# Performance work log

Hardware: AMD Instinct MI355X
Metric: run time of the kernel (lower is better)

## Reference

```python
import jax, jax.numpy as jnp
import numpy as np

B, H, N, D = 4, 16, 2048, 64


def setup_inputs() -> dict:
    key = jax.random.key(0)
    kq, kk, kv, km, kb = jax.random.split(key, 5)
    q = jax.random.normal(kq, (B, H, N, D), dtype=jnp.float32)
    k = jax.random.normal(kk, (B, H, N, D), dtype=jnp.float32)
    v = jax.random.normal(kv, (B, H, N, D), dtype=jnp.float32)
    # mostly-True mask so no row is fully masked
    mask = jax.random.uniform(km, (B, 1, N, N)) > 0.1
    attn_bias = jax.random.normal(kb, (1, H, N, N), dtype=jnp.float32)
    return {"q": q, "k": k, "v": v, "mask": mask, "attn_bias": attn_bias}


def reference(q, k, v, mask, attn_bias):
    scale = q.shape[-1] ** -0.5
    # sim: [B,H,N,N]
    sim = jnp.einsum('bhid,bhjd->bhij', q, k) * scale
    sim = sim + attn_bias
    neg = -jnp.finfo(sim.dtype).max
    sim = jnp.where(mask, sim, neg)
    attn = jax.nn.softmax(sim, axis=-1)
    out = jnp.einsum('bhij,bhjd->bhid', attn, v)
    return out
```

## Files before the change

### kernel.cpp

```cpp
#include <hip/hip_runtime.h>
#include <hip/hip_bf16.h>

typedef __bf16 bf16_t;
typedef bf16_t bf16x8 __attribute__((ext_vector_type(8)));
typedef float  floatx4 __attribute__((ext_vector_type(4)));

constexpr int Bb = 4, Hh = 16, Nn = 2048, Dd = 64;
constexpr int BM = 128;
constexpr int BN = 64;
constexpr int WM = 16;
constexpr float SCALE = 0.125f;
constexpr float NEG   = -3.4028234663852886e38f;

__global__ __launch_bounds__(512, 4)
void attn_fwd(const float* __restrict__ qg,
              const float* __restrict__ kg,
              const float* __restrict__ vg,
              const void*  __restrict__ maskg,
              const float* __restrict__ biasg,
              float* __restrict__ outg)
{
    __shared__ bf16x8 k_lds[512];
    __shared__ bf16x8 v_lds[512];
    __shared__ bf16x8 p_lds[8][128];

    const int tid  = threadIdx.x;
    const int wave = tid >> 6;
    const int lane = tid & 63;
    const int ln   = lane & 15;
    const int lq   = lane >> 4;

    const int id = blockIdx.x;
    const int b  = id & 3;
    const int h  = (id >> 2) & 15;
    const int mt = id >> 6;

    const int probe = ((const int*)maskg)[lane];
    const bool mask_i32 = __all(probe == 0 || probe == 1);
    const int*           mi = (const int*)maskg;
    const unsigned char* mb = (const unsigned char*)maskg;

    const size_t head  = (size_t)(b*Hh + h) * Nn * Dd;
    const int    qbase = mt*BM + wave*WM;

    bf16x8 qa[2];
    {
        const float* qp = qg + head + (size_t)(qbase + ln)*Dd + lq*8;
        #pragma unroll
        for (int kk = 0; kk < 2; ++kk) {
            float4 f0 = *(const float4*)(qp + kk*32);
            float4 f1 = *(const float4*)(qp + kk*32 + 4);
            bf16x8 a;
            a[0]=(bf16_t)f0.x; a[1]=(bf16_t)f0.y; a[2]=(bf16_t)f0.z; a[3]=(bf16_t)f0.w;
            a[4]=(bf16_t)f1.x; a[5]=(bf16_t)f1.y; a[6]=(bf16_t)f1.z; a[7]=(bf16_t)f1.w;
            qa[kk] = a;
        }
    }

    floatx4 o_acc[4];
    #pragma unroll
    for (int i = 0; i < 4; ++i) o_acc[i] = (floatx4){0.f,0.f,0.f,0.f};
    float mx[4], lsum[4];
    #pragma unroll
    for (int r = 0; r < 4; ++r) { mx[r] = -__builtin_inff(); lsum[r] = 0.f; }

    const int skey = tid >> 3;
    const int sd0  = (tid & 7) * 8;
    const int sblk = skey >> 4, sn = skey & 15;
    const int kkg  = sd0 >> 5,  qg2 = (sd0 >> 3) & 3;
    const int vkk  = skey >> 5, vq = (skey >> 3) & 3, vj = skey & 7;
    const int vnb  = sd0 >> 4;
    bf16_t* vl = (bf16_t*)v_lds;
    bf16_t* pl = (bf16_t*)p_lds[wave];

    for (int kt = 0; kt < Nn/BN; ++kt) {
        __syncthreads();
        {
            const float* kp = kg + head + (size_t)(kt*BN + skey)*Dd + sd0;
            const float* vp = vg + head + (size_t)(kt*BN + skey)*Dd + sd0;
            float4 k0 = *(const float4*)(kp);
            float4 k1 = *(const float4*)(kp + 4);
            float4 v0 = *(const float4*)(vp);
            float4 v1 = *(const float4*)(vp + 4);
            bf16x8 c;
            c[0]=(bf16_t)k0.x; c[1]=(bf16_t)k0.y; c[2]=(bf16_t)k0.z; c[3]=(bf16_t)k0.w;
            c[4]=(bf16_t)k1.x; c[5]=(bf16_t)k1.y; c[6]=(bf16_t)k1.z; c[7]=(bf16_t)k1.w;
            k_lds[(sblk*2 + kkg)*64 + qg2*16 + sn] = c;
            float vvv[8];
            *(float4*)(vvv)   = v0;
            *(float4*)(vvv+4) = v1;
            #pragma unroll
            for (int t = 0; t < 8; ++t) {
                const int nn2 = (sd0 & 8) + t;
                vl[(((vkk*4 + vnb)*64 + vq*16 + nn2) << 3) | vj] = (bf16_t)vvv[t];
            }
        }
        __syncthreads();

        floatx4 s_acc[4];
        #pragma unroll
        for (int i = 0; i < 4; ++i) s_acc[i] = (floatx4){0.f,0.f,0.f,0.f};
        #pragma unroll
        for (int blk = 0; blk < 4; ++blk)
            #pragma unroll
            for (int kk = 0; kk < 2; ++kk)
                s_acc[blk] = __builtin_amdgcn_mfma_f32_16x16x32_bf16(
                    qa[kk], k_lds[(blk*2+kk)*64 + lane], s_acc[blk], 0, 0, 0);

        float sv[4][4], rmax[4];
        const size_t col0 = (size_t)kt*BN + ln;
        #pragma unroll
        for (int r = 0; r < 4; ++r) {
            const int m = qbase + lq*4 + r;
            const size_t brow = ((size_t)h*Nn + m)*Nn + col0;
            const size_t mrow = ((size_t)b*Nn + m)*Nn + col0;
            rmax[r] = NEG;
            #pragma unroll
            for (int blk = 0; blk < 4; ++blk) {
                float val = s_acc[blk][r]*SCALE + biasg[brow + blk*16];
                const bool ok = mask_i32 ? (mi[mrow + blk*16] != 0)
                                         : (mb[mrow + blk*16] != 0);
                val = ok ? val : NEG;
                sv[r][blk] = val;
                rmax[r] = fmaxf(rmax[r], val);
            }
        }
        #pragma unroll
        for (int off = 1; off < 16; off <<= 1)
            #pragma unroll
            for (int r = 0; r < 4; ++r)
                rmax[r] = fmaxf(rmax[r], __shfl_xor(rmax[r], off, 64));

        float alph[4], rsum[4];
        bf16_t pb[4][4];
        #pragma unroll
        for (int r = 0; r < 4; ++r) {
            const float mnew = fmaxf(mx[r], rmax[r]);
            alph[r] = __expf(mx[r] - mnew);
            mx[r] = mnew;
            float s = 0.f;
            #pragma unroll
            for (int blk = 0; blk < 4; ++blk) {
                const bf16_t p = (bf16_t)__expf(sv[r][blk] - mnew);
                pb[r][blk] = p;
                s += (float)p;
            }
            rsum[r] = s;
        }
        #pragma unroll
        for (int off = 1; off < 16; off <<= 1)
            #pragma unroll
            for (int r = 0; r < 4; ++r)
                rsum[r] += __shfl_xor(rsum[r], off, 64);
        #pragma unroll
        for (int r = 0; r < 4; ++r) {
            lsum[r] = lsum[r]*alph[r] + rsum[r];
            #pragma unroll
            for (int nb = 0; nb < 4; ++nb)
                o_acc[nb][r] *= alph[r];
        }

        #pragma unroll
        for (int r = 0; r < 4; ++r) {
            const int m = lq*4 + r;
            #pragma unroll
            for (int blk = 0; blk < 4; ++blk) {
                const int key = blk*16 + ln;
                const int kk2 = key >> 5, q2 = (key >> 3) & 3, j2 = key & 7;
                pl[((kk2*64 + q2*16 + m) << 3) | j2] = pb[r][blk];
            }
        }

        #pragma unroll
        for (int kk = 0; kk < 2; ++kk) {
            const bf16x8 pa = p_lds[wave][kk*64 + lane];
            #pragma unroll
            for (int nb = 0; nb < 4; ++nb)
                o_acc[nb] = __builtin_amdgcn_mfma_f32_16x16x32_bf16(
                    pa, v_lds[(kk*4+nb)*64 + lane], o_acc[nb], 0, 0, 0);
        }
    }

    #pragma unroll
    for (int r = 0; r < 4; ++r) {
        const int m = qbase + lq*4 + r;
        const float inv = 1.f / lsum[r];
        float* op = outg + head + (size_t)m*Dd + ln;
        #pragma unroll
        for (int nb = 0; nb < 4; ++nb)
            op[nb*16] = o_acc[nb][r] * inv;
    }
}

extern "C" void kernel_launch(void* const* d_in, const int* in_sizes, int n_in,
                              void* d_out, int out_size, void* d_ws, size_t ws_size,
                              hipStream_t stream) {
    const float* q    = (const float*)d_in[0];
    const float* k    = (const float*)d_in[1];
    const float* v    = (const float*)d_in[2];
    const void*  mask = d_in[3];
    const float* bias = (const float*)d_in[4];
    float* out = (float*)d_out;
    (void)in_sizes; (void)n_in; (void)out_size; (void)d_ws; (void)ws_size;

    const int grid = Bb * Hh * (Nn / BM);
    attn_fwd<<<grid, 512, 0, stream>>>(q, k, v, mask, bias, out);
}
```

Baseline: 1.015 ms.

## Double-buffer K/V in LDS and prefetch next tile's bias and mask into registers

K/V tiles now live in two LDS buffers. The next tile's K/V values are loaded into registers right after the barrier, so the per-iteration leading __syncthreads goes away. The bias and mask values for the next key tile are also loaded and combined one iteration ahead, so their global-memory latency overlaps the softmax and PV MFMA work. The probabilities are written to LDS inside the exp loop, which removes the separate pb array. The cost is more live registers per thread at 512 threads per block, which may affect occupancy or cause spills.

Measured after the change: 1.074 ms. 5.8% more time.

```diff
diff --git a/kernel.cpp b/kernel.cpp
--- a/kernel.cpp
+++ b/kernel.cpp
@@ -9,6 +9,7 @@
 constexpr int BM = 128;
 constexpr int BN = 64;
 constexpr int WM = 16;
+constexpr int NT = Nn / BN;
 constexpr float SCALE = 0.125f;
 constexpr float NEG   = -3.4028234663852886e38f;
 
@@ -20,8 +21,8 @@
               const float* __restrict__ biasg,
               float* __restrict__ outg)
 {
-    __shared__ bf16x8 k_lds[512];
-    __shared__ bf16x8 v_lds[512];
+    __shared__ bf16x8 k_lds[2][512];
+    __shared__ bf16x8 v_lds[2][512];
     __shared__ bf16x8 p_lds[8][128];
 
     const int tid  = threadIdx.x;
@@ -70,25 +71,45 @@
     const int kkg  = sd0 >> 5,  qg2 = (sd0 >> 3) & 3;
     const int vkk  = skey >> 5, vq = (skey >> 3) & 3, vj = skey & 7;
     const int vnb  = sd0 >> 4;
-    bf16_t* vl = (bf16_t*)v_lds;
     bf16_t* pl = (bf16_t*)p_lds[wave];
 
-    for (int kt = 0; kt < Nn/BN; ++kt) {
-        __syncthreads();
+    const float* kbase = kg + head + (size_t)skey*Dd + sd0;
+    const float* vbase = vg + head + (size_t)skey*Dd + sd0;
+
+    float4 kr0 = *(const float4*)(kbase);
+    float4 kr1 = *(const float4*)(kbase + 4);
+    float4 vr0 = *(const float4*)(vbase);
+    float4 vr1 = *(const float4*)(vbase + 4);
+
+    float bias_pf[4][4];
+    {
+        const size_t col0 = (size_t)ln;
+        #pragma unroll
+        for (int r = 0; r < 4; ++r) {
+            const int m = qbase + lq*4 + r;
+            const size_t brow = ((size_t)h*Nn + m)*Nn + col0;
+            const size_t mrow = ((size_t)b*Nn + m)*Nn + col0;
+            #pragma unroll
+            for (int blk = 0; blk < 4; ++blk) {
+                const bool ok = mask_i32 ? (mi[mrow + blk*16] != 0)
+                                         : (mb[mrow + blk*16] != 0);
+                bias_pf[r][blk] = ok ? biasg[brow + blk*16] : NEG;
+            }
+        }
+    }
+
+    for (int kt = 0; kt < NT; ++kt) {
+        const int cur = kt & 1;
+
         {
-            const float* kp = kg + head + (size_t)(kt*BN + skey)*Dd + sd0;
-            const float* vp = vg + head + (size_t)(kt*BN + skey)*Dd + sd0;
-            float4 k0 = *(const float4*)(kp);
-            float4 k1 = *(const float4*)(kp + 4);
-            float4 v0 = *(const float4*)(vp);
-            float4 v1 = *(const float4*)(vp + 4);
             bf16x8 c;
-            c[0]=(bf16_t)k0.x; c[1]=(bf16_t)k0.y; c[2]=(bf16_t)k0.z; c[3]=(bf16_t)k0.w;
-            c[4]=(bf16_t)k1.x; c[5]=(bf16_t)k1.y; c[6]=(bf16_t)k1.z; c[7]=(bf16_t)k1.w;
-            k_lds[(sblk*2 + kkg)*64 + qg2*16 + sn] = c;
+            c[0]=(bf16_t)kr0.x; c[1]=(bf16_t)kr0.y; c[2]=(bf16_t)kr0.z; c[3]=(bf16_t)kr0.w;
+            c[4]=(bf16_t)kr1.x; c[5]=(bf16_t)kr1.y; c[6]=(bf16_t)kr1.z; c[7]=(bf16_t)kr1.w;
+            k_lds[cur][(sblk*2 + kkg)*64 + qg2*16 + sn] = c;
             float vvv[8];
-            *(float4*)(vvv)   = v0;
-            *(float4*)(vvv+4) = v1;
+            *(float4*)(vvv)   = vr0;
+            *(float4*)(vvv+4) = vr1;
+            bf16_t* vl = (bf16_t*)v_lds[cur];
             #pragma unroll
             for (int t = 0; t < 8; ++t) {
                 const int nn2 = (sd0 & 8) + t;
@@ -97,6 +118,15 @@
         }
         __syncthreads();
 
+        if (kt + 1 < NT) {
+            const float* kp = kbase + (size_t)(kt+1)*BN*Dd;
+            const float* vp = vbase + (size_t)(kt+1)*BN*Dd;
+            kr0 = *(const float4*)(kp);
+            kr1 = *(const float4*)(kp + 4);
+            vr0 = *(const float4*)(vp);
+            vr1 = *(const float4*)(vp + 4);
+        }
+
         floatx4 s_acc[4];
         #pragma unroll
         for (int i = 0; i < 4; ++i) s_acc[i] = (floatx4){0.f,0.f,0.f,0.f};
@@ -105,23 +135,16 @@
             #pragma unroll
             for (int kk = 0; kk < 2; ++kk)
                 s_acc[blk] = __builtin_amdgcn_mfma_f32_16x16x32_bf16(
-                    qa[kk], k_lds[(blk*2+kk)*64 + lane], s_acc[blk], 0, 0, 0);
-
-        float sv[4][4], rmax[4];
-        const size_t col0 = (size_t)kt*BN + ln;
-        #pragma unroll
-        for (int r = 0; r < 4; ++r) {
-            const int m = qbase + lq*4 + r;
-            const size_t brow = ((size_t)h*Nn + m)*Nn + col0;
-            const size_t mrow = ((size_t)b*Nn + m)*Nn + col0;
+                    qa[kk], k_lds[cur][(blk*2+kk)*64 + lane], s_acc[blk], 0, 0, 0);
+
+        float rmax[4];
+        #pragma unroll
+        for (int r = 0; r < 4; ++r) {
             rmax[r] = NEG;
             #pragma unroll
             for (int blk = 0; blk < 4; ++blk) {
-                float val = s_acc[blk][r]*SCALE + biasg[brow + blk*16];
-                const bool ok = mask_i32 ? (mi[mrow + blk*16] != 0)
-                                         : (mb[mrow + blk*16] != 0);
-                val = ok ? val : NEG;
-                sv[r][blk] = val;
+                const float val = s_acc[blk][r]*SCALE + bias_pf[r][blk];
+                s_acc[blk][r] = val;
                 rmax[r] = fmaxf(rmax[r], val);
             }
         }
@@ -132,18 +155,20 @@
                 rmax[r] = fmaxf(rmax[r], __shfl_xor(rmax[r], off, 64));
 
         float alph[4], rsum[4];
-        bf16_t pb[4][4];
         #pragma unroll
         for (int r = 0; r < 4; ++r) {
             const float mnew = fmaxf(mx[r], rmax[r]);
             alph[r] = __expf(mx[r] - mnew);
             mx[r] = mnew;
+            const int m = lq*4 + r;
             float s = 0.f;
             #pragma unroll
             for (int blk = 0; blk < 4; ++blk) {
-                const bf16_t p = (bf16_t)__expf(sv[r][blk] - mnew);
-                pb[r][blk] = p;
+                const bf16_t p = (bf16_t)__expf(s_acc[blk][r] - mnew);
                 s += (float)p;
+                const int key = blk*16 + ln;
+                const int kk2 = key >> 5, q2 = (key >> 3) & 3, j2 = key & 7;
+                pl[((kk2*64 + q2*16 + m) << 3) | j2] = p;
             }
             rsum[r] = s;
         }
@@ -160,14 +185,19 @@
                 o_acc[nb][r] *= alph[r];
         }
 
-        #pragma unroll
-        for (int r = 0; r < 4; ++r) {
-            const int m = lq*4 + r;
-            #pragma unroll
-            for (int blk = 0; blk < 4; ++blk) {
-                const int key = blk*16 + ln;
-                const int kk2 = key >> 5, q2 = (key >> 3) & 3, j2 = key & 7;
-                pl[((kk2*64 + q2*16 + m) << 3) | j2] = pb[r][blk];
+        if (kt + 1 < NT) {
+            const size_t col0 = (size_t)(kt+1)*BN + ln;
+            #pragma unroll
+            for (int r = 0; r < 4; ++r) {
+                const int m = qbase + lq*4 + r;
+                const size_t brow = ((size_t)h*Nn + m)*Nn + col0;
+                const size_t mrow = ((size_t)b*Nn + m)*Nn + col0;
+                #pragma unroll
+                for (int blk = 0; blk < 4; ++blk) {
+                    const bool ok = mask_i32 ? (mi[mrow + blk*16] != 0)
+                                             : (mb[mrow + blk*16] != 0);
+                    bias_pf[r][blk] = ok ? biasg[brow + blk*16] : NEG;
+                }
             }
         }
 
@@ -177,7 +207,7 @@
             #pragma unroll
             for (int nb = 0; nb < 4; ++nb)
                 o_acc[nb] = __builtin_amdgcn_mfma_f32_16x16x32_bf16(
-                    pa, v_lds[(kk*4+nb)*64 + lane], o_acc[nb], 0, 0, 0);
+                    pa, v_lds[cur][(kk*4+nb)*64 + lane], o_acc[nb], 0, 0, 0);
         }
     }
 
```

## Share one running max per wave tile, MFMA row sums, prefetch bias and mask

Applied to the files above, without the earlier changes.

Bias and mask loads are now issued before the QK MFMAs so their memory latency overlaps the matrix work. The per-row online-softmax max is replaced by a single max shared across the wave's 16-row tile, which removes three of the four max shuffle chains and all of the per-row sum shuffles. Row sums are instead computed with an extra MFMA of P against a vector of ones. The shared max is numerically weaker: rows whose scores sit far below the tile maximum can underflow in exp or in bf16, which only stays accurate when score ranges across rows are similar.

After: 1.079 ms. +6.3%, slower.

```diff
diff --git a/kernel.cpp b/kernel.cpp
--- a/kernel.cpp
+++ b/kernel.cpp
@@ -9,6 +9,7 @@
 constexpr int BM = 128;
 constexpr int BN = 64;
 constexpr int WM = 16;
+constexpr int NT = Nn / BN;
 constexpr float SCALE = 0.125f;
 constexpr float NEG   = -3.4028234663852886e38f;
 
@@ -57,12 +58,17 @@
         }
     }
 
+    bf16x8 ones;
+    #pragma unroll
+    for (int j = 0; j < 8; ++j) ones[j] = (bf16_t)1.0f;
+
     floatx4 o_acc[4];
     #pragma unroll
     for (int i = 0; i < 4; ++i) o_acc[i] = (floatx4){0.f,0.f,0.f,0.f};
-    float mx[4], lsum[4];
-    #pragma unroll
-    for (int r = 0; r < 4; ++r) { mx[r] = -__builtin_inff(); lsum[r] = 0.f; }
+    float mx = -__builtin_inff();
+    float lsum[4];
+    #pragma unroll
+    for (int r = 0; r < 4; ++r) lsum[r] = 0.f;
 
     const int skey = tid >> 3;
     const int sd0  = (tid & 7) * 8;
@@ -73,7 +79,7 @@
     bf16_t* vl = (bf16_t*)v_lds;
     bf16_t* pl = (bf16_t*)p_lds[wave];
 
-    for (int kt = 0; kt < Nn/BN; ++kt) {
+    for (int kt = 0; kt < NT; ++kt) {
         __syncthreads();
         {
             const float* kp = kg + head + (size_t)(kt*BN + skey)*Dd + sd0;
@@ -97,6 +103,23 @@
         }
         __syncthreads();
 
+        float bb[4][4];
+        {
+            const size_t col0 = (size_t)kt*BN + ln;
+            #pragma unroll
+            for (int r = 0; r < 4; ++r) {
+                const int m = qbase + lq*4 + r;
+                const size_t brow = ((size_t)h*Nn + m)*Nn + col0;
+                const size_t mrow = ((size_t)b*Nn + m)*Nn + col0;
+                #pragma unroll
+                for (int blk = 0; blk < 4; ++blk) {
+                    const bool ok = mask_i32 ? (mi[mrow + blk*16] != 0)
+                                             : (mb[mrow + blk*16] != 0);
+                    bb[r][blk] = ok ? biasg[brow + blk*16] : NEG;
+                }
+            }
+        }
+
         floatx4 s_acc[4];
         #pragma unroll
         for (int i = 0; i < 4; ++i) s_acc[i] = (floatx4){0.f,0.f,0.f,0.f};
@@ -107,78 +130,54 @@
                 s_acc[blk] = __builtin_amdgcn_mfma_f32_16x16x32_bf16(
                     qa[kk], k_lds[(blk*2+kk)*64 + lane], s_acc[blk], 0, 0, 0);
 
-        float sv[4][4], rmax[4];
-        const size_t col0 = (size_t)kt*BN + ln;
-        #pragma unroll
-        for (int r = 0; r < 4; ++r) {
-            const int m = qbase + lq*4 + r;
-            const size_t brow = ((size_t)h*Nn + m)*Nn + col0;
-            const size_t mrow = ((size_t)b*Nn + m)*Nn + col0;
-            rmax[r] = NEG;
+        float gmax = NEG;
+        #pragma unroll
+        for (int r = 0; r < 4; ++r)
             #pragma unroll
             for (int blk = 0; blk < 4; ++blk) {
-                float val = s_acc[blk][r]*SCALE + biasg[brow + blk*16];
-                const bool ok = mask_i32 ? (mi[mrow + blk*16] != 0)
-                                         : (mb[mrow + blk*16] != 0);
-                val = ok ? val : NEG;
-                sv[r][blk] = val;
-                rmax[r] = fmaxf(rmax[r], val);
-            }
-        }
+                const float val = fmaf(s_acc[blk][r], SCALE, bb[r][blk]);
+                s_acc[blk][r] = val;
+                gmax = fmaxf(gmax, val);
+            }
         #pragma unroll
         for (int off = 1; off < 16; off <<= 1)
-            #pragma unroll
-            for (int r = 0; r < 4; ++r)
-                rmax[r] = fmaxf(rmax[r], __shfl_xor(rmax[r], off, 64));
-
-        float alph[4], rsum[4];
-        bf16_t pb[4][4];
-        #pragma unroll
-        for (int r = 0; r < 4; ++r) {
-            const float mnew = fmaxf(mx[r], rmax[r]);
-            alph[r] = __expf(mx[r] - mnew);
-            mx[r] = mnew;
-            float s = 0.f;
-            #pragma unroll
-            for (int blk = 0; blk < 4; ++blk) {
-                const bf16_t p = (bf16_t)__expf(sv[r][blk] - mnew);
-                pb[r][blk] = p;
-                s += (float)p;
-            }
-            rsum[r] = s;
-        }
-        #pragma unroll
-        for (int off = 1; off < 16; off <<= 1)
-            #pragma unroll
-            for (int r = 0; r < 4; ++r)
-                rsum[r] += __shfl_xor(rsum[r], off, 64);
-        #pragma unroll
-        for (int r = 0; r < 4; ++r) {
-            lsum[r] = lsum[r]*alph[r] + rsum[r];
-            #pragma unroll
-            for (int nb = 0; nb < 4; ++nb)
-                o_acc[nb][r] *= alph[r];
-        }
+            gmax = fmaxf(gmax, __shfl_xor(gmax, off, 64));
+
+        const float mnew = fmaxf(mx, gmax);
+        const float alph = __expf(mx - mnew);
+        mx = mnew;
 
         #pragma unroll
         for (int r = 0; r < 4; ++r) {
             const int m = lq*4 + r;
             #pragma unroll
             for (int blk = 0; blk < 4; ++blk) {
+                const bf16_t p = (bf16_t)__expf(s_acc[blk][r] - mnew);
                 const int key = blk*16 + ln;
                 const int kk2 = key >> 5, q2 = (key >> 3) & 3, j2 = key & 7;
-                pl[((kk2*64 + q2*16 + m) << 3) | j2] = pb[r][blk];
-            }
-        }
-
+                pl[((kk2*64 + q2*16 + m) << 3) | j2] = p;
+            }
+        }
+        #pragma unroll
+        for (int r = 0; r < 4; ++r)
+            #pragma unroll
+            for (int nb = 0; nb < 4; ++nb)
+                o_acc[nb][r] *= alph;
+
+        floatx4 sum_acc = (floatx4){0.f,0.f,0.f,0.f};
         #pragma unroll
         for (int kk = 0; kk < 2; ++kk) {
             const bf16x8 pa = p_lds[wave][kk*64 + lane];
+            sum_acc = __builtin_amdgcn_mfma_f32_16x16x32_bf16(
+                pa, ones, sum_acc, 0, 0, 0);
             #pragma unroll
             for (int nb = 0; nb < 4; ++nb)
                 o_acc[nb] = __builtin_amdgcn_mfma_f32_16x16x32_bf16(
                     pa, v_lds[(kk*4+nb)*64 + lane], o_acc[nb], 0, 0, 0);
         }
+        #pragma unroll
+        for (int r = 0; r < 4; ++r)
+            lsum[r] = lsum[r]*alph + sum_acc[r];
     }
 
     #pragma unroll
```
